# Kernel tuning notes

Measured on AMD Instinct MI355X. Metric: run time of the kernel, lower is better.

The kernel has to match this reference:

```python
import jax, jax.numpy as jnp
import numpy as np


def setup_inputs() -> dict:
    key = jax.random.key(0)
    k1, k2, k3, k4 = jax.random.split(key, 4)
    N, T, F = 8192, 128, 9
    M_s = 256
    merged = jax.random.normal(k1, (N, T, F), dtype=jnp.float32)
    input1 = jax.random.normal(k2, (N, T, F), dtype=jnp.float32)
    samples = jax.random.normal(k3, (N, M_s), dtype=jnp.float32)
    labels = jax.random.randint(k4, (N,), 0, 10, dtype=jnp.int32)
    return {"merged": merged, "input1": input1, "samples": samples, "labels": labels}


def reference(merged, input1, samples, labels):
    # Pairwise squared distances S_ij = sum_k (s_i - s_j)^2 / M_s, computed via
    # the Gram-matrix identity instead of materializing the [N, N, M_s] tensor.
    M_s = samples.shape[1]
    sq = jnp.sum(samples * samples, axis=-1)                 # [N]
    gram = jnp.einsum('im,jm->ij', samples, samples)         # [N, N]
    S_ij = (sq[:, None] + sq[None, :] - 2.0 * gram) / jnp.float32(M_s)
    same = (labels[:, None] == labels[None, :]).astype(jnp.float32)
    term2 = jnp.mean(jnp.maximum(0.0, (1.0 - same) * (1.0 - S_ij)))
    L_label = 10.0 * jnp.mean(same * S_ij) + 10.0 * term2
    return L_label
```

## Files before the change

kernel.cpp:

```cpp
#include <hip/hip_runtime.h>
#include <hip/hip_bf16.h>

#define NROWS 8192
#define KDIM  256
#define NT    64
#define NBLK  (NT * (NT + 1) / 2)
#define GRID  512

typedef __attribute__((ext_vector_type(4))) float f32x4;

#define GLD(gp, lp)                                                            \
  __builtin_amdgcn_global_load_lds(                                            \
      (const __attribute__((address_space(1))) void*)(gp),                     \
      (__attribute__((address_space(3))) void*)(lp), 16, 0, 0)

__global__ void prep_kernel(const float* __restrict__ samples,
                            unsigned char* __restrict__ sf8,
                            float* __restrict__ sq,
                            float* __restrict__ accg) {
  int t = threadIdx.x, lane = t & 63, wv = t >> 6;
  int row = blockIdx.x * 4 + wv;
  float4 v = ((const float4*)samples)[(size_t)row * 64 + lane];
  int pk0 = __builtin_amdgcn_cvt_pk_fp8_f32(v.x, v.y, 0, false);
  int pk1 = __builtin_amdgcn_cvt_pk_fp8_f32(v.z, v.w, 0, false);
  ((unsigned int*)sf8)[(size_t)row * 64 + lane] =
      (unsigned)(pk0 & 0xffff) | ((unsigned)pk1 << 16);
  float p = v.x * v.x + v.y * v.y + v.z * v.z + v.w * v.w;
#pragma unroll
  for (int off = 32; off; off >>= 1) p += __shfl_down(p, off);
  if (lane == 0) sq[row] = p;
  if (row == 0 && lane < 2) accg[lane] = 0.0f;
}

__device__ inline void decode_tile(int b, int& bi, int& bj) {
  float disc = (2.0f * NT + 1.0f) * (2.0f * NT + 1.0f) - 8.0f * (float)b;
  bi = (int)(((2.0f * NT + 1.0f) - sqrtf(disc)) * 0.5f);
  if (bi < 0) bi = 0;
  if (bi > NT - 1) bi = NT - 1;
  while (bi > 0 && (bi * NT - bi * (bi - 1) / 2) > b) --bi;
  while (((bi + 1) * NT - (bi + 1) * bi / 2) <= b) ++bi;
  bj = bi + (b - (bi * NT - bi * (bi - 1) / 2));
}

__global__ __launch_bounds__(512, 4) void pair_kernel(
    const unsigned char* __restrict__ sf8, const float* __restrict__ sq,
    const int* __restrict__ labels, float* __restrict__ accg) {

  __shared__ __align__(16) unsigned char Bs[2][32 * 1024];
  __shared__ float red[16];

  int t = threadIdx.x;
  int lane = t & 63;
  int w = t >> 6;
  int wm = w >> 1, wn = w & 1;
  int lr = lane >> 4, pc = lane & 15;
  int r = lane & 15;
  int ko = lane >> 4;
  int kq = ko >> 1, hf = (ko & 1) * 8;
  int q4 = ko * 4;

  int t0 = (blockIdx.x * 65) >> 4;
  int t1 = ((blockIdx.x + 1) * 65) >> 4;
  int bi, bj;
  decode_tile(t0, bi, bj);

  long af[2][8];
  float sqa[8];
  int laa[8];
  auto loadA = [&](int bi_) {
#pragma unroll
    for (int i = 0; i < 2; i++) {
      const unsigned char* Ar =
          sf8 + (size_t)(bi_ * 128 + wm * 32 + i * 16 + r) * KDIM + ko * 8;
#pragma unroll
      for (int kc = 0; kc < 8; kc++) af[i][kc] = *(const long*)(Ar + kc * 32);
    }
#pragma unroll
    for (int i = 0; i < 2; i++)
#pragma unroll
      for (int q = 0; q < 4; q++) {
        int gr = bi_ * 128 + wm * 32 + i * 16 + q4 + q;
        sqa[i * 4 + q] = sq[gr];
        laa[i * 4 + q] = labels[gr];
      }
  };

  auto stageB = [&](int bj_, int buf) {
#pragma unroll
    for (int p = 0; p < 4; ++p) {
      int region = p * 8 + w;
      int rr = region * 4 + lr;
      int c = pc ^ (rr & 15);
      GLD(sf8 + (size_t)(bj_ * 128 + rr) * KDIM + c * 16,
          &Bs[buf][region * 1024]);
    }
  };

  int abi = bi;
  loadA(bi);
  stageB(bj, 0);
  int cur = 0;
  float s1t = 0.f, s2t = 0.f;

  for (int tile = t0; tile < t1; ++tile) {
    __syncthreads();

    float sqb[4];
    int lab[4];
#pragma unroll
    for (int j = 0; j < 4; j++) {
      int gc = bj * 128 + wn * 64 + j * 16 + r;
      sqb[j] = sq[gc];
      lab[j] = labels[gc];
    }

    if (bi != abi) { loadA(bi); abi = bi; }

    int nbi = bi, nbj = bj + 1;
    if (nbj == NT) { ++nbi; nbj = nbi; }
    if (tile + 1 < t1) stageB(nbj, cur ^ 1);

    f32x4 acc[2][4];
#pragma unroll
    for (int i = 0; i < 2; i++)
#pragma unroll
      for (int j = 0; j < 4; j++) acc[i][j] = (f32x4){0.f, 0.f, 0.f, 0.f};

#pragma unroll
    for (int kc = 0; kc < 8; ++kc) {
      long bfr[4];
#pragma unroll
      for (int j = 0; j < 4; j++) {
        int n = wn * 64 + j * 16 + r;
        bfr[j] =
            *(const long*)(&Bs[cur][n * 256 + (((kc * 2 + kq) ^ r) * 16) + hf]);
      }
#pragma unroll
      for (int i = 0; i < 2; i++)
#pragma unroll
        for (int j = 0; j < 4; j++)
          acc[i][j] = __builtin_amdgcn_mfma_f32_16x16x32_fp8_fp8(
              af[i][kc], bfr[j], acc[i][j], 0, 0, 0);
    }

    float s1 = 0.f, s2 = 0.f;
#pragma unroll
    for (int j = 0; j < 4; j++) {
#pragma unroll
      for (int i = 0; i < 2; i++) {
#pragma unroll
        for (int q = 0; q < 4; q++) {
          float S = (sqa[i * 4 + q] + sqb[j] - 2.0f * acc[i][j][q]) *
                    (1.0f / 256.0f);
          if (laa[i * 4 + q] == lab[j]) s1 += S;
          else                          s2 += fmaxf(0.f, 1.f - S);
        }
      }
    }
    float wt = (bi == bj) ? 1.0f : 2.0f;
    s1t += wt * s1;
    s2t += wt * s2;

    bi = nbi; bj = nbj; cur ^= 1;
  }

#pragma unroll
  for (int off = 32; off; off >>= 1) {
    s1t += __shfl_down(s1t, off);
    s2t += __shfl_down(s2t, off);
  }
  if (lane == 0) { red[w] = s1t; red[8 + w] = s2t; }
  __syncthreads();
  if (t == 0) {
    float a = 0.f, b2 = 0.f;
#pragma unroll
    for (int k = 0; k < 8; k++) { a += red[k]; b2 += red[8 + k]; }
    atomicAdd(&accg[0], a);
    atomicAdd(&accg[1], b2);
  }
}

__global__ void finalize_kernel(const float* __restrict__ accg,
                                float* __restrict__ out) {
  out[0] = 10.0f * (accg[0] + accg[1]) *
           (1.0f / ((float)NROWS * (float)NROWS));
}

extern "C" void kernel_launch(void* const* d_in, const int* in_sizes, int n_in,
                              void* d_out, int out_size, void* d_ws,
                              size_t ws_size, hipStream_t stream) {
  const float* samples = (const float*)d_in[2];
  const int*   labels  = (const int*)d_in[3];

  char* ws = (char*)d_ws;
  unsigned char* sf8 = (unsigned char*)ws;
  float* sq   = (float*)(ws + (size_t)NROWS * KDIM);
  float* accg = (float*)(ws + (size_t)NROWS * KDIM + NROWS * 4);
  float* out  = (float*)d_out;

  prep_kernel<<<NROWS / 4, 256, 0, stream>>>(samples, sf8, sq, accg);
  pair_kernel<<<GRID, 512, 0, stream>>>(sf8, sq, labels, accg);
  finalize_kernel<<<1, 1, 0, stream>>>(accg, out);
}
```

Before: 153.0 us.

## Launch one 256-thread block per upper-triangle tile instead of persistent loop

Replaces the persistent grid of 512 blocks, each looping over about 4 tiles with double-buffered LDS staging, with one block per 128x128 upper-triangular tile (2080 blocks, 4 waves each). Each wave now covers 32 rows by 128 columns, and the B tile is staged once with no prefetch loop. The aim is to drop the inter-tile loop and the double buffer, letting the hardware scheduler overlap blocks and balance the load across CUs. In exchange, each block reloads A, sq and labels, and the per-block atomics to the global accumulator grow from 512 to 2080.

```diff
diff --git a/kernel.cpp b/kernel.cpp
--- a/kernel.cpp
+++ b/kernel.cpp
@@ -5,7 +5,6 @@
 #define KDIM  256
 #define NT    64
 #define NBLK  (NT * (NT + 1) / 2)
-#define GRID  512
 
 typedef __attribute__((ext_vector_type(4))) float f32x4;
 
@@ -42,141 +41,111 @@
   bj = bi + (b - (bi * NT - bi * (bi - 1) / 2));
 }
 
-__global__ __launch_bounds__(512, 4) void pair_kernel(
+__global__ __launch_bounds__(256) void pair_kernel(
     const unsigned char* __restrict__ sf8, const float* __restrict__ sq,
     const int* __restrict__ labels, float* __restrict__ accg) {
 
-  __shared__ __align__(16) unsigned char Bs[2][32 * 1024];
-  __shared__ float red[16];
+  __shared__ __align__(16) unsigned char Bs[32 * 1024];
 
   int t = threadIdx.x;
   int lane = t & 63;
   int w = t >> 6;
-  int wm = w >> 1, wn = w & 1;
-  int lr = lane >> 4, pc = lane & 15;
+  int lr4 = lane >> 4, pc = lane & 15;
   int r = lane & 15;
   int ko = lane >> 4;
   int kq = ko >> 1, hf = (ko & 1) * 8;
   int q4 = ko * 4;
 
-  int t0 = (blockIdx.x * 65) >> 4;
-  int t1 = ((blockIdx.x + 1) * 65) >> 4;
   int bi, bj;
-  decode_tile(t0, bi, bj);
+  decode_tile((int)blockIdx.x, bi, bj);
+  int rowA0 = bi * 128, rowB0 = bj * 128;
+
+#pragma unroll
+  for (int p = 0; p < 8; ++p) {
+    int region = w * 8 + p;
+    int rr = region * 4 + lr4;
+    int c = pc ^ (rr & 15);
+    GLD(sf8 + (size_t)(rowB0 + rr) * KDIM + c * 16, &Bs[region * 1024]);
+  }
 
   long af[2][8];
+#pragma unroll
+  for (int i = 0; i < 2; i++) {
+    const unsigned char* Ar =
+        sf8 + (size_t)(rowA0 + w * 32 + i * 16 + r) * KDIM + ko * 8;
+#pragma unroll
+    for (int kc = 0; kc < 8; kc++) af[i][kc] = *(const long*)(Ar + kc * 32);
+  }
   float sqa[8];
   int laa[8];
-  auto loadA = [&](int bi_) {
 #pragma unroll
-    for (int i = 0; i < 2; i++) {
-      const unsigned char* Ar =
-          sf8 + (size_t)(bi_ * 128 + wm * 32 + i * 16 + r) * KDIM + ko * 8;
+  for (int i = 0; i < 2; i++)
 #pragma unroll
-      for (int kc = 0; kc < 8; kc++) af[i][kc] = *(const long*)(Ar + kc * 32);
+    for (int q = 0; q < 4; q++) {
+      int gr = rowA0 + w * 32 + i * 16 + q4 + q;
+      sqa[i * 4 + q] = sq[gr];
+      laa[i * 4 + q] = labels[gr];
+    }
+  float sqb[8];
+  int lab[8];
+#pragma unroll
+  for (int j = 0; j < 8; j++) {
+    int gc = rowB0 + j * 16 + r;
+    sqb[j] = sq[gc];
+    lab[j] = labels[gc];
+  }
+
+  __syncthreads();
+
+  f32x4 acc[2][8];
+#pragma unroll
+  for (int i = 0; i < 2; i++)
+#pragma unroll
+    for (int j = 0; j < 8; j++) acc[i][j] = (f32x4){0.f, 0.f, 0.f, 0.f};
+
+#pragma unroll
+  for (int kc = 0; kc < 8; ++kc) {
+    long bfr[8];
+#pragma unroll
+    for (int j = 0; j < 8; j++) {
+      bfr[j] = *(const long*)(&Bs[(j * 16 + r) * 256 +
+                                  (((kc * 2 + kq) ^ r) * 16) + hf]);
     }
 #pragma unroll
     for (int i = 0; i < 2; i++)
 #pragma unroll
+      for (int j = 0; j < 8; j++)
+        acc[i][j] = __builtin_amdgcn_mfma_f32_16x16x32_fp8_fp8(
+            af[i][kc], bfr[j], acc[i][j], 0, 0, 0);
+  }
+
+  float s1 = 0.f, s2 = 0.f;
+#pragma unroll
+  for (int j = 0; j < 8; j++) {
+#pragma unroll
+    for (int i = 0; i < 2; i++) {
+#pragma unroll
       for (int q = 0; q < 4; q++) {
-        int gr = bi_ * 128 + wm * 32 + i * 16 + q4 + q;
-        sqa[i * 4 + q] = sq[gr];
-        laa[i * 4 + q] = labels[gr];
-      }
-  };
-
-  auto stageB = [&](int bj_, int buf) {
-#pragma unroll
-    for (int p = 0; p < 4; ++p) {
-      int region = p * 8 + w;
-      int rr = region * 4 + lr;
-      int c = pc ^ (rr & 15);
-      GLD(sf8 + (size_t)(bj_ * 128 + rr) * KDIM + c * 16,
-          &Bs[buf][region * 1024]);
-    }
-  };
-
-  int abi = bi;
-  loadA(bi);
-  stageB(bj, 0);
-  int cur = 0;
-  float s1t = 0.f, s2t = 0.f;
-
-  for (int tile = t0; tile < t1; ++tile) {
-    __syncthreads();
-
-    float sqb[4];
-    int lab[4];
-#pragma unroll
-    for (int j = 0; j < 4; j++) {
-      int gc = bj * 128 + wn * 64 + j * 16 + r;
-      sqb[j] = sq[gc];
-      lab[j] = labels[gc];
-    }
-
-    if (bi != abi) { loadA(bi); abi = bi; }
-
-    int nbi = bi, nbj = bj + 1;
-    if (nbj == NT) { ++nbi; nbj = nbi; }
-    if (tile + 1 < t1) stageB(nbj, cur ^ 1);
-
-    f32x4 acc[2][4];
-#pragma unroll
-    for (int i = 0; i < 2; i++)
-#pragma unroll
-      for (int j = 0; j < 4; j++) acc[i][j] = (f32x4){0.f, 0.f, 0.f, 0.f};
-
-#pragma unroll
-    for (int kc = 0; kc < 8; ++kc) {
-      long bfr[4];
-#pragma unroll
-      for (int j = 0; j < 4; j++) {
-        int n = wn * 64 + j * 16 + r;
-        bfr[j] =
-            *(const long*)(&Bs[cur][n * 256 + (((kc * 2 + kq) ^ r) * 16) + hf]);
-      }
-#pragma unroll
-      for (int i = 0; i < 2; i++)
-#pragma unroll
-        for (int j = 0; j < 4; j++)
-          acc[i][j] = __builtin_amdgcn_mfma_f32_16x16x32_fp8_fp8(
-              af[i][kc], bfr[j], acc[i][j], 0, 0, 0);
-    }
-
-    float s1 = 0.f, s2 = 0.f;
-#pragma unroll
-    for (int j = 0; j < 4; j++) {
-#pragma unroll
-      for (int i = 0; i < 2; i++) {
-#pragma unroll
-        for (int q = 0; q < 4; q++) {
-          float S = (sqa[i * 4 + q] + sqb[j] - 2.0f * acc[i][j][q]) *
-                    (1.0f / 256.0f);
-          if (laa[i * 4 + q] == lab[j]) s1 += S;
-          else                          s2 += fmaxf(0.f, 1.f - S);
-        }
+        float S = (sqa[i * 4 + q] + sqb[j] - 2.0f * acc[i][j][q]) *
+                  (1.0f / 256.0f);
+        if (laa[i * 4 + q] == lab[j]) s1 += S;
+        else                          s2 += fmaxf(0.f, 1.f - S);
       }
     }
-    float wt = (bi == bj) ? 1.0f : 2.0f;
-    s1t += wt * s1;
-    s2t += wt * s2;
-
-    bi = nbi; bj = nbj; cur ^= 1;
   }
-
 #pragma unroll
   for (int off = 32; off; off >>= 1) {
-    s1t += __shfl_down(s1t, off);
-    s2t += __shfl_down(s2t, off);
+    s1 += __shfl_down(s1, off);
+    s2 += __shfl_down(s2, off);
   }
-  if (lane == 0) { red[w] = s1t; red[8 + w] = s2t; }
+  __syncthreads();
+  float* red = (float*)&Bs[0];
+  if (lane == 0) { red[w] = s1; red[4 + w] = s2; }
   __syncthreads();
   if (t == 0) {
-    float a = 0.f, b2 = 0.f;
-#pragma unroll
-    for (int k = 0; k < 8; k++) { a += red[k]; b2 += red[8 + k]; }
-    atomicAdd(&accg[0], a);
-    atomicAdd(&accg[1], b2);
+    float wt = (bi == bj) ? 1.0f : 2.0f;
+    atomicAdd(&accg[0], (red[0] + red[1] + red[2] + red[3]) * wt);
+    atomicAdd(&accg[1], (red[4] + red[5] + red[6] + red[7]) * wt);
   }
 }
 
@@ -199,6 +168,6 @@
   float* out  = (float*)d_out;
 
   prep_kernel<<<NROWS / 4, 256, 0, stream>>>(samples, sf8, sq, accg);
-  pair_kernel<<<GRID, 512, 0, stream>>>(sf8, sq, labels, accg);
+  pair_kernel<<<NBLK, 256, 0, stream>>>(sf8, sq, labels, accg);
   finalize_kernel<<<1, 1, 0, stream>>>(accg, out);
 }
```

After: 163.6 us. 1.07x slower.
